# Kernel tuning notes

Measured on AMD Instinct MI355X. Metric: run time of the kernel, lower is better.

## Reference

```python
import jax, jax.numpy as jnp
import numpy as np

N_NODES = 50000
NEG_SLOPE = 0.2

def _gat_conv(x, W, att_src, att_dst, bias, src, dst):
    # x: [N, in_c] -> h: [N, out_c]
    h = x @ W
    a_src = (h * att_src).sum(-1)  # [N]
    a_dst = (h * att_dst).sum(-1)  # [N]
    e = a_src[src] + a_dst[dst]    # [E]
    e = jnp.where(e > 0, e, NEG_SLOPE * e)  # LeakyReLU
    # segment softmax over destination node neighborhoods
    emax = jax.ops.segment_max(e, dst, num_segments=N_NODES)
    ee = jnp.exp(e - emax[dst])
    denom = jax.ops.segment_sum(ee, dst, num_segments=N_NODES)
    alpha = ee / denom[dst]        # [E]
    out = jax.ops.segment_sum(h[src] * alpha[:, None], dst, num_segments=N_NODES)
    return out + bias

def _with_self_loops(edge_index):
    # PyG GATConv default add_self_loops=True
    loop = jnp.arange(N_NODES, dtype=edge_index.dtype)
    src = jnp.concatenate([edge_index[0], loop])
    dst = jnp.concatenate([edge_index[1], loop])
    return src, dst

def setup_inputs() -> dict:
    key = jax.random.key(0)
    ks = jax.random.split(key, 11)
    in_c, hid_c, out_c = 256, 128, 64
    E = 800000
    x = jax.random.normal(ks[0], (N_NODES, in_c), dtype=jnp.float32)
    edge_index = jax.random.randint(ks[1], (2, E), 0, N_NODES, dtype=jnp.int64)
    s1 = 1.0 / np.sqrt(in_c)
    s2 = 1.0 / np.sqrt(hid_c)
    return {
        "x": x,
        "edge_index": edge_index,
        "W1": jax.random.normal(ks[2], (in_c, hid_c), dtype=jnp.float32) * s1,
        "att_src1": jax.random.normal(ks[3], (hid_c,), dtype=jnp.float32) * s2,
        "att_dst1": jax.random.normal(ks[4], (hid_c,), dtype=jnp.float32) * s2,
        "b1": jax.random.normal(ks[5], (hid_c,), dtype=jnp.float32) * 0.01,
        "W2": jax.random.normal(ks[6], (hid_c, out_c), dtype=jnp.float32) * s2,
        "att_src2": jax.random.normal(ks[7], (out_c,), dtype=jnp.float32) * (1.0 / np.sqrt(out_c)),
        "att_dst2": jax.random.normal(ks[8], (out_c,), dtype=jnp.float32) * (1.0 / np.sqrt(out_c)),
        "b2": jax.random.normal(ks[9], (out_c,), dtype=jnp.float32) * 0.01,
    }

def reference(x, edge_index, W1, att_src1, att_dst1, b1, W2, att_src2, att_dst2, b2):
    src, dst = _with_self_loops(edge_index)
    hid = _gat_conv(x, W1, att_src1, att_dst1, b1, src, dst)
    hid = jax.nn.relu(hid)
    out = _gat_conv(hid, W2, att_src2, att_dst2, b2, src, dst)
    return jax.nn.log_softmax(out, axis=1)
```

## Files before the change

kernel.cpp:

```cpp
#include <hip/hip_runtime.h>
#include <hip/hip_bf16.h>
#include <math.h>

#define N_NODES 50000
#define E_RAW   800000
#define E_TOT   850000
#define NEG_SLOPE 0.2f
#define CAP 64

typedef __attribute__((ext_vector_type(8))) short short8;
typedef __attribute__((ext_vector_type(4))) float f32x4;

__device__ __forceinline__ short f2bf(float f) {
    __hip_bfloat16 h = __float2bfloat16(f);
    return *reinterpret_cast<short*>(&h);
}
__device__ __forceinline__ unsigned int f2bfu(float f) {
    __hip_bfloat16 h = __float2bfloat16(f);
    return (unsigned int)*reinterpret_cast<unsigned short*>(&h);
}
__device__ __forceinline__ float bflo(unsigned int u) {
    return __uint_as_float(u << 16);
}
__device__ __forceinline__ float bfhi(unsigned int u) {
    return __uint_as_float(u & 0xffff0000u);
}

template<int K, int N>
__global__ __launch_bounds__(256) void gat_wf_kernel(
        const float* __restrict__ W, short* __restrict__ Wf) {
    constexpr int NT = N / 16;
    const int idx = blockIdx.x * 256 + threadIdx.x;
    if (idx >= K * N) return;
    const int j  = idx & 7;
    const int n  = (idx >> 3) & 15;
    const int q  = (idx >> 7) & 3;
    const int t  = (idx >> 9) % NT;
    const int kc = idx / (512 * NT);
    const int k   = kc * 32 + q * 8 + j;
    const int col = t * 16 + n;
    Wf[idx] = f2bf(W[(size_t)k * N + col]);
}

template<int K, int N, bool BF16_IN>
__device__ __forceinline__ void gemm_att_body(
        const int blk,
        const float* __restrict__ xf, const short* __restrict__ xb,
        const short* __restrict__ Wf,
        const float* __restrict__ att_src, const float* __restrict__ att_dst,
        short* __restrict__ h_bf,
        float* __restrict__ a_src, float* __restrict__ a_dst) {
    constexpr int NT = N / 16;
    constexpr int KC = K / 32;
    const int tid  = threadIdx.x;
    const int lane = tid & 63;
    const int wv   = tid >> 6;
    const int mrow = lane & 15;
    const int q    = lane >> 4;

    const int row0 = blk * 64 + wv * 16;
    const int rowA = row0 + mrow;
    const int rowAc = rowA < N_NODES ? rowA : 0;

    f32x4 acc[NT];
    #pragma unroll
    for (int t = 0; t < NT; ++t) acc[t] = f32x4{0.f, 0.f, 0.f, 0.f};

    #pragma unroll
    for (int kc = 0; kc < KC; ++kc) {
        short8 a;
        if (BF16_IN) {
            a = *(const short8*)&xb[(size_t)rowAc * K + kc * 32 + q * 8];
        } else {
            const float4 f0 = *(const float4*)&xf[(size_t)rowAc * K + kc * 32 + q * 8];
            const float4 f1 = *(const float4*)&xf[(size_t)rowAc * K + kc * 32 + q * 8 + 4];
            a[0] = f2bf(f0.x); a[1] = f2bf(f0.y); a[2] = f2bf(f0.z); a[3] = f2bf(f0.w);
            a[4] = f2bf(f1.x); a[5] = f2bf(f1.y); a[6] = f2bf(f1.z); a[7] = f2bf(f1.w);
        }
        #pragma unroll
        for (int t = 0; t < NT; ++t) {
            const short8 b = *(const short8*)&Wf[((size_t)(kc * NT + t) * 64 + lane) * 8];
            acc[t] = __builtin_amdgcn_mfma_f32_16x16x32_bf16(a, b, acc[t], 0, 0, 0);
        }
    }

    #pragma unroll
    for (int r = 0; r < 4; ++r) {
        const int rowD = row0 + q * 4 + r;
        float ps = 0.0f, pd = 0.0f;
        #pragma unroll
        for (int t = 0; t < NT; ++t) {
            const int col = t * 16 + mrow;
            ps = fmaf(acc[t][r], att_src[col], ps);
            pd = fmaf(acc[t][r], att_dst[col], pd);
        }
        #pragma unroll
        for (int off = 8; off > 0; off >>= 1) {
            ps += __shfl_xor(ps, off);
            pd += __shfl_xor(pd, off);
        }
        if (rowD < N_NODES) {
            if (mrow == 0) { a_src[rowD] = ps; a_dst[rowD] = pd; }
            #pragma unroll
            for (int t = 0; t < NT; ++t)
                h_bf[(size_t)rowD * N + t * 16 + mrow] = f2bf(acc[t][r]);
        }
    }
}

template<int K, int N>
__global__ __launch_bounds__(256) void gat_fat1_kernel(
        const float* __restrict__ xf, const short* __restrict__ Wf,
        const float* __restrict__ att_src, const float* __restrict__ att_dst,
        short* __restrict__ h_bf,
        float* __restrict__ a_src, float* __restrict__ a_dst,
        const int* __restrict__ ei, int* __restrict__ cnt,
        int* __restrict__ srcs, int GB) {
    if ((int)blockIdx.x < GB) {
        gemm_att_body<K, N, false>(blockIdx.x, xf, nullptr, Wf,
                                   att_src, att_dst, h_bf, a_src, a_dst);
    } else {
        const int i = (blockIdx.x - GB) * 256 + threadIdx.x;
        if (i >= E_TOT) return;
        int s, d;
        if (i < E_RAW) { s = ei[i]; d = ei[E_RAW + i]; }
        else           { s = d = i - E_RAW; }
        const int c = atomicAdd(&cnt[d], 1);
        if (c < CAP) srcs[(d << 6) + c] = s;
    }
}

template<int K, int N, bool BF16_IN>
__global__ __launch_bounds__(256) void gat_gemm_att_kernel(
        const float* __restrict__ xf, const short* __restrict__ xb,
        const short* __restrict__ Wf,
        const float* __restrict__ att_src, const float* __restrict__ att_dst,
        short* __restrict__ h_bf,
        float* __restrict__ a_src, float* __restrict__ a_dst) {
    gemm_att_body<K, N, BF16_IN>(blockIdx.x, xf, xb, Wf,
                                 att_src, att_dst, h_bf, a_src, a_dst);
}

template<int N, bool RELU, bool LSM, bool OUT_BF16>
__global__ __launch_bounds__(256) void gat_aggr_kernel(
        const int* __restrict__ cnt, const int* __restrict__ srcs,
        const float* __restrict__ a_src, const float* __restrict__ a_dst,
        const unsigned short* __restrict__ h_bf, const float* __restrict__ bias,
        float* __restrict__ outf, uint4* __restrict__ outb) {
    constexpr int EPL = N / 16;
    const int lane = threadIdx.x & 63;
    const int wave = threadIdx.x >> 6;
    const int d = blockIdx.x * 4 + wave;
    if (d >= N_NODES) return;
    const int beg = d << 6;
    int deg = cnt[d];
    deg = deg < CAP ? deg : CAP;
    const float ad = a_dst[d];

    const int sreg = srcs[beg + (lane < deg ? lane : 0)];
    float e;
    if (lane < deg) {
        float t = a_src[sreg] + ad;
        e = t > 0.0f ? t : NEG_SLOPE * t;
    } else {
        e = -1e30f;
    }
    float m = e;
    #pragma unroll
    for (int off = 32; off > 0; off >>= 1) m = fmaxf(m, __shfl_xor(m, off));
    const float anum = __expf(e - m);
    float ss = anum;
    #pragma unroll
    for (int off = 32; off > 0; off >>= 1) ss += __shfl_xor(ss, off);
    const float areg = anum / ss;

    const int g   = lane >> 4;
    const int sub = lane & 15;
    float acc[EPL];
    #pragma unroll
    for (int c = 0; c < EPL; ++c) acc[c] = 0.0f;

    for (int j = 0; j < deg; j += 4) {
        const int eidx = j + g;
        const int s    = __shfl(sreg, eidx);
        float alpha    = __shfl(areg, eidx);
        if (eidx >= deg) alpha = 0.0f;
        const unsigned short* hp = h_bf + (size_t)s * N + sub * EPL;
        if (EPL == 8) {
            const uint4 hv = *(const uint4*)hp;
            acc[0] = fmaf(alpha, bflo(hv.x), acc[0]);
            acc[1] = fmaf(alpha, bfhi(hv.x), acc[1]);
            acc[2] = fmaf(alpha, bflo(hv.y), acc[2]);
            acc[3] = fmaf(alpha, bfhi(hv.y), acc[3]);
            acc[4] = fmaf(alpha, bflo(hv.z), acc[4]);
            acc[5] = fmaf(alpha, bfhi(hv.z), acc[5]);
            acc[6] = fmaf(alpha, bflo(hv.w), acc[6]);
            acc[7] = fmaf(alpha, bfhi(hv.w), acc[7]);
        } else {
            const uint2 hv = *(const uint2*)hp;
            acc[0] = fmaf(alpha, bflo(hv.x), acc[0]);
            acc[1] = fmaf(alpha, bfhi(hv.x), acc[1]);
            acc[2] = fmaf(alpha, bflo(hv.y), acc[2]);
            acc[3] = fmaf(alpha, bfhi(hv.y), acc[3]);
        }
    }

    #pragma unroll
    for (int c = 0; c < EPL; ++c) {
        acc[c] += __shfl_xor(acc[c], 16);
        acc[c] += __shfl_xor(acc[c], 32);
    }

    if (LSM) {
        float v[4];
        #pragma unroll
        for (int c = 0; c < 4; ++c) v[c] = acc[c] + bias[sub * 4 + c];
        float mm = fmaxf(fmaxf(v[0], v[1]), fmaxf(v[2], v[3]));
        #pragma unroll
        for (int off = 1; off < 16; off <<= 1) mm = fmaxf(mm, __shfl_xor(mm, off));
        float es = __expf(v[0] - mm) + __expf(v[1] - mm)
                 + __expf(v[2] - mm) + __expf(v[3] - mm);
        #pragma unroll
        for (int off = 1; off < 16; off <<= 1) es += __shfl_xor(es, off);
        const float ls = logf(es);
        if (lane < 16) {
            float4 o;
            o.x = v[0] - mm - ls; o.y = v[1] - mm - ls;
            o.z = v[2] - mm - ls; o.w = v[3] - mm - ls;
            *(float4*)&outf[(size_t)d * N + sub * 4] = o;
        }
    } else {
        if (lane < 16) {
            const float4 b0 = *(const float4*)&bias[sub * 8];
            const float4 b1 = *(const float4*)&bias[sub * 8 + 4];
            float v[8];
            v[0] = acc[0] + b0.x; v[1] = acc[1] + b0.y;
            v[2] = acc[2] + b0.z; v[3] = acc[3] + b0.w;
            v[4] = acc[4] + b1.x; v[5] = acc[5] + b1.y;
            v[6] = acc[6] + b1.z; v[7] = acc[7] + b1.w;
            if (RELU)
                #pragma unroll
                for (int c = 0; c < 8; ++c) v[c] = fmaxf(v[c], 0.0f);
            uint4 p;
            p.x = f2bfu(v[0]) | (f2bfu(v[1]) << 16);
            p.y = f2bfu(v[2]) | (f2bfu(v[3]) << 16);
            p.z = f2bfu(v[4]) | (f2bfu(v[5]) << 16);
            p.w = f2bfu(v[6]) | (f2bfu(v[7]) << 16);
            outb[(size_t)d * (N / 8) + sub] = p;
        }
    }
}

extern "C" void kernel_launch(void* const* d_in, const int* in_sizes, int n_in,
                              void* d_out, int out_size, void* d_ws, size_t ws_size,
                              hipStream_t stream) {
    const float* x        = (const float*)d_in[0];
    const int*   ei       = (const int*)  d_in[1];
    const float* W1       = (const float*)d_in[2];
    const float* att_src1 = (const float*)d_in[3];
    const float* att_dst1 = (const float*)d_in[4];
    const float* b1       = (const float*)d_in[5];
    const float* W2       = (const float*)d_in[6];
    const float* att_src2 = (const float*)d_in[7];
    const float* att_dst2 = (const float*)d_in[8];
    const float* b2       = (const float*)d_in[9];
    float* out = (float*)d_out;
    float* ws  = (float*)d_ws;

    float* a_src1 = ws;
    float* a_dst1 = a_src1 + 50000;
    float* a_src2 = a_dst1 + 50000;
    float* a_dst2 = a_src2 + 50000;
    int*   cnt    = (int*)(a_dst2 + 50000);
    int*   srcs   = cnt + 50000;
    short* hbf1   = (short*)(srcs + 50000 * CAP);
    short* agg1b  = hbf1  + 6400000;
    short* Wf1    = agg1b + 6400000;
    short* Wf2    = Wf1   + 32768;
    short* hbf2   = hbf1;

    hipMemsetAsync(cnt, 0, (size_t)50000 * 4, stream);

    const int EB = (E_TOT + 255) / 256;
    const int GB = (N_NODES + 63) / 64;

    gat_wf_kernel<256, 128><<<128, 256, 0, stream>>>(W1, Wf1);
    gat_wf_kernel<128, 64><<<32, 256, 0, stream>>>(W2, Wf2);

    gat_fat1_kernel<256, 128><<<GB + EB, 256, 0, stream>>>(
        x, Wf1, att_src1, att_dst1, hbf1, a_src1, a_dst1,
        ei, cnt, srcs, GB);

    gat_aggr_kernel<128, true, false, true><<<12500, 256, 0, stream>>>(
        cnt, srcs, a_src1, a_dst1, (const unsigned short*)hbf1, b1,
        nullptr, (uint4*)agg1b);

    gat_gemm_att_kernel<128, 64, true><<<GB, 256, 0, stream>>>(
        nullptr, agg1b, Wf2, att_src2, att_dst2, hbf2, a_src2, a_dst2);
    gat_aggr_kernel<64, false, true, false><<<12500, 256, 0, stream>>>(
        cnt, srcs, a_src2, a_dst2, (const unsigned short*)hbf2, b2,
        out, nullptr);
}
```

Baseline: 245.9 us.

## Prefetch neighbor rows in aggregation, merge weight prep, reorder fused edge/GEMM blocks

```diff
diff --git a/kernel.cpp b/kernel.cpp
--- a/kernel.cpp
+++ b/kernel.cpp
@@ -27,10 +27,10 @@
 }
 
 template<int K, int N>
-__global__ __launch_bounds__(256) void gat_wf_kernel(
-        const float* __restrict__ W, short* __restrict__ Wf) {
+__device__ __forceinline__ void wf_body(
+        int blk, const float* __restrict__ W, short* __restrict__ Wf) {
     constexpr int NT = N / 16;
-    const int idx = blockIdx.x * 256 + threadIdx.x;
+    const int idx = blk * 256 + threadIdx.x;
     if (idx >= K * N) return;
     const int j  = idx & 7;
     const int n  = (idx >> 3) & 15;
@@ -40,6 +40,14 @@
     const int k   = kc * 32 + q * 8 + j;
     const int col = t * 16 + n;
     Wf[idx] = f2bf(W[(size_t)k * N + col]);
+}
+
+__global__ __launch_bounds__(256) void gat_wf2x_kernel(
+        const float* __restrict__ W1, short* __restrict__ Wf1,
+        const float* __restrict__ W2, short* __restrict__ Wf2) {
+    const int b = blockIdx.x;
+    if (b < 128) wf_body<256, 128>(b, W1, Wf1);
+    else         wf_body<128, 64>(b - 128, W2, Wf2);
 }
 
 template<int K, int N, bool BF16_IN>
@@ -115,18 +123,23 @@
         short* __restrict__ h_bf,
         float* __restrict__ a_src, float* __restrict__ a_dst,
         const int* __restrict__ ei, int* __restrict__ cnt,
-        int* __restrict__ srcs, int GB) {
-    if ((int)blockIdx.x < GB) {
-        gemm_att_body<K, N, false>(blockIdx.x, xf, nullptr, Wf,
+        int* __restrict__ srcs, int EB) {
+    if ((int)blockIdx.x >= EB) {
+        gemm_att_body<K, N, false>(blockIdx.x - EB, xf, nullptr, Wf,
                                    att_src, att_dst, h_bf, a_src, a_dst);
     } else {
-        const int i = (blockIdx.x - GB) * 256 + threadIdx.x;
-        if (i >= E_TOT) return;
-        int s, d;
-        if (i < E_RAW) { s = ei[i]; d = ei[E_RAW + i]; }
-        else           { s = d = i - E_RAW; }
-        const int c = atomicAdd(&cnt[d], 1);
-        if (c < CAP) srcs[(d << 6) + c] = s;
+        const int i0 = blockIdx.x * 512 + threadIdx.x;
+        #pragma unroll
+        for (int u = 0; u < 2; ++u) {
+            const int i = i0 + u * 256;
+            if (i < E_TOT) {
+                int s, d;
+                if (i < E_RAW) { s = ei[i]; d = ei[E_RAW + i]; }
+                else           { s = d = i - E_RAW; }
+                const int c = atomicAdd(&cnt[d], 1);
+                if (c < CAP) srcs[(d << 6) + c] = s;
+            }
+        }
     }
 }
 
@@ -141,7 +154,7 @@
                                  att_src, att_dst, h_bf, a_src, a_dst);
 }
 
-template<int N, bool RELU, bool LSM, bool OUT_BF16>
+template<int N, bool LSM>
 __global__ __launch_bounds__(256) void gat_aggr_kernel(
         const int* __restrict__ cnt, const int* __restrict__ srcs,
         const float* __restrict__ a_src, const float* __restrict__ a_dst,
@@ -180,14 +193,28 @@
     #pragma unroll
     for (int c = 0; c < EPL; ++c) acc[c] = 0.0f;
 
+    int eidx = g;
+    int ec = eidx < deg ? eidx : 0;
+    int s = __shfl(sreg, ec);
+    float alpha = __shfl(areg, ec);
+    if (eidx >= deg) alpha = 0.0f;
+    uint4 hv;
+    uint2 hv2;
+    if (EPL == 8) hv  = *(const uint4*)(h_bf + (size_t)s * N + sub * 8);
+    else          hv2 = *(const uint2*)(h_bf + (size_t)s * N + sub * 4);
+
     for (int j = 0; j < deg; j += 4) {
-        const int eidx = j + g;
-        const int s    = __shfl(sreg, eidx);
-        float alpha    = __shfl(areg, eidx);
-        if (eidx >= deg) alpha = 0.0f;
-        const unsigned short* hp = h_bf + (size_t)s * N + sub * EPL;
+        const int eidxn = j + 4 + g;
+        const int ecn = eidxn < deg ? eidxn : 0;
+        const int sn = __shfl(sreg, ecn);
+        float alphan = __shfl(areg, ecn);
+        if (eidxn >= deg) alphan = 0.0f;
+        uint4 hvn;
+        uint2 hv2n;
+        if (EPL == 8) hvn  = *(const uint4*)(h_bf + (size_t)sn * N + sub * 8);
+        else          hv2n = *(const uint2*)(h_bf + (size_t)sn * N + sub * 4);
+
         if (EPL == 8) {
-            const uint4 hv = *(const uint4*)hp;
             acc[0] = fmaf(alpha, bflo(hv.x), acc[0]);
             acc[1] = fmaf(alpha, bfhi(hv.x), acc[1]);
             acc[2] = fmaf(alpha, bflo(hv.y), acc[2]);
@@ -197,12 +224,12 @@
             acc[6] = fmaf(alpha, bflo(hv.w), acc[6]);
             acc[7] = fmaf(alpha, bfhi(hv.w), acc[7]);
         } else {
-            const uint2 hv = *(const uint2*)hp;
-            acc[0] = fmaf(alpha, bflo(hv.x), acc[0]);
-            acc[1] = fmaf(alpha, bfhi(hv.x), acc[1]);
-            acc[2] = fmaf(alpha, bflo(hv.y), acc[2]);
-            acc[3] = fmaf(alpha, bfhi(hv.y), acc[3]);
-        }
+            acc[0] = fmaf(alpha, bflo(hv2.x), acc[0]);
+            acc[1] = fmaf(alpha, bfhi(hv2.x), acc[1]);
+            acc[2] = fmaf(alpha, bflo(hv2.y), acc[2]);
+            acc[3] = fmaf(alpha, bfhi(hv2.y), acc[3]);
+        }
+        hv = hvn; hv2 = hv2n; alpha = alphan;
     }
 
     #pragma unroll
@@ -238,15 +265,14 @@
             v[2] = acc[2] + b0.z; v[3] = acc[3] + b0.w;
             v[4] = acc[4] + b1.x; v[5] = acc[5] + b1.y;
             v[6] = acc[6] + b1.z; v[7] = acc[7] + b1.w;
-            if (RELU)
-                #pragma unroll
-                for (int c = 0; c < 8; ++c) v[c] = fmaxf(v[c], 0.0f);
+            #pragma unroll
+            for (int c = 0; c < 8; ++c) v[c] = fmaxf(v[c], 0.0f);
             uint4 p;
             p.x = f2bfu(v[0]) | (f2bfu(v[1]) << 16);
             p.y = f2bfu(v[2]) | (f2bfu(v[3]) << 16);
             p.z = f2bfu(v[4]) | (f2bfu(v[5]) << 16);
             p.w = f2bfu(v[6]) | (f2bfu(v[7]) << 16);
-            outb[(size_t)d * (N / 8) + sub] = p;
+            outb[(size_t)d * 16 + sub] = p;
         }
     }
 }
@@ -281,23 +307,22 @@
 
     hipMemsetAsync(cnt, 0, (size_t)50000 * 4, stream);
 
-    const int EB = (E_TOT + 255) / 256;
+    const int EB = (E_TOT + 511) / 512;
     const int GB = (N_NODES + 63) / 64;
 
-    gat_wf_kernel<256, 128><<<128, 256, 0, stream>>>(W1, Wf1);
-    gat_wf_kernel<128, 64><<<32, 256, 0, stream>>>(W2, Wf2);
-
-    gat_fat1_kernel<256, 128><<<GB + EB, 256, 0, stream>>>(
+    gat_wf2x_kernel<<<160, 256, 0, stream>>>(W1, Wf1, W2, Wf2);
+
+    gat_fat1_kernel<256, 128><<<EB + GB, 256, 0, stream>>>(
         x, Wf1, att_src1, att_dst1, hbf1, a_src1, a_dst1,
-        ei, cnt, srcs, GB);
-
-    gat_aggr_kernel<128, true, false, true><<<12500, 256, 0, stream>>>(
+        ei, cnt, srcs, EB);
+
+    gat_aggr_kernel<128, false><<<12500, 256, 0, stream>>>(
         cnt, srcs, a_src1, a_dst1, (const unsigned short*)hbf1, b1,
         nullptr, (uint4*)agg1b);
 
     gat_gemm_att_kernel<128, 64, true><<<GB, 256, 0, stream>>>(
         nullptr, agg1b, Wf2, att_src2, att_dst2, hbf2, a_src2, a_dst2);
-    gat_aggr_kernel<64, false, true, false><<<12500, 256, 0, stream>>>(
+    gat_aggr_kernel<64, true><<<12500, 256, 0, stream>>>(
         cnt, srcs, a_src2, a_dst2, (const unsigned short*)hbf2, b2,
         out, nullptr);
 }
```

After: 261.0 us. 1.06x slower.
